# Optimization experiments

Hardware: AMD Instinct MI355X
Metric: run time of the kernel (lower is better)

## Reference

```python
import jax, jax.numpy as jnp
import numpy as np

B, S, HID = 128, 512, 512
IN_DIM = 1  # forced by x[:, t].unsqueeze(-1) + cat along dim 2


def setup_inputs() -> dict:
    key = jax.random.key(0)
    ks = jax.random.split(key, 9)
    scale = 0.05
    d_in = IN_DIM + HID
    return {
        "x": jax.random.normal(ks[0], (B, S, IN_DIM), dtype=jnp.float32),
        "H_prev": jnp.zeros((B, 1, HID), dtype=jnp.float32),
        "C_prev": jnp.zeros((B, 1, HID), dtype=jnp.float32),
        "Wi": jax.random.normal(ks[1], (d_in, HID), dtype=jnp.float32) * scale,
        "bi": jax.random.normal(ks[2], (1, HID), dtype=jnp.float32) * scale,
        "Wf": jax.random.normal(ks[3], (d_in, HID), dtype=jnp.float32) * scale,
        "bf": jax.random.normal(ks[4], (1, HID), dtype=jnp.float32) * scale,
        "Wc": jax.random.normal(ks[5], (d_in, HID), dtype=jnp.float32) * scale,
        "bc": jax.random.normal(ks[6], (1, HID), dtype=jnp.float32) * scale,
        "Wo": jax.random.normal(ks[7], (d_in, HID), dtype=jnp.float32) * scale,
        "bo": jax.random.normal(ks[8], (1, HID), dtype=jnp.float32) * scale,
    }


def reference(x, H_prev, C_prev, Wi, bi, Wf, bf, Wc, bc, Wo, bo):
    # x: [B, S, 1]; H_prev, C_prev: [B, 1, HID]
    def step(carry, x_t):
        H, C = carry  # each [B, 1, HID]
        comb = jnp.concatenate([x_t[:, None, :], H], axis=2)  # [B, 1, 1+HID]
        I = jax.nn.sigmoid(comb @ Wi + bi)
        F = jax.nn.sigmoid(comb @ Wf + bf)
        C_hat = jnp.tanh(comb @ Wc + bc)
        O = comb @ Wo + bo  # NOTE: no sigmoid, faithful to source
        C_new = F * C + I * C_hat
        H_new = O * jnp.tanh(C_new)
        return (H_new, C_new), None

    xs = jnp.swapaxes(x, 0, 1)  # [S, B, 1]
    (H_t, C_t), _ = jax.lax.scan(step, (H_prev, C_prev), xs)
    # original returns (hidden_sequence, H_t, C_t) where hidden_sequence == last H_t
    return (H_t, H_t, C_t)
```

## Files before the change

### kernel.cpp

```cpp
#include <hip/hip_runtime.h>
#include <math.h>

#define SEQ 512
#define HID 512
#define NGROUP 8
#define GB 16
#define BPG 32
#define SLOTU 65536
#define GSLOTU 8192
#define LROW 520

typedef __attribute__((ext_vector_type(8))) short short8;
typedef __attribute__((ext_vector_type(4))) float floatx4;

__device__ __forceinline__ unsigned short f2bf(float f) {
    unsigned u = __builtin_bit_cast(unsigned, f);
    return (unsigned short)((u + 0x7FFFu + ((u >> 16) & 1u)) >> 16);
}
__device__ __forceinline__ float bf2f(unsigned short h) {
    unsigned u = ((unsigned)h) << 16;
    return __builtin_bit_cast(float, u);
}
__device__ __forceinline__ float fast_sigmoid(float x) {
    return 1.0f / (1.0f + __expf(-x));
}
__device__ __forceinline__ float fast_tanh(float x) {
    float e = __expf(-2.0f * fabsf(x));
    float t = (1.0f - e) / (1.0f + e);
    return x < 0.0f ? -t : t;
}

__global__ void lstm_init(const float* __restrict__ H0, unsigned short* __restrict__ hb) {
    int idx = blockIdx.x * blockDim.x + threadIdx.x;
    if (idx < SLOTU) {
        int k = idx & 511, b = (idx >> 9) & 15, g = idx >> 13;
        hb[idx] = f2bf(H0[(g * GB + b) * HID + k]);
    } else if (idx < SLOTU + NGROUP * 64) {
        ((int*)(hb + 2 * SLOTU))[idx - SLOTU] = 0;
    }
}

__global__ __launch_bounds__(256, 1)
void lstm_main(const float* __restrict__ x,
               const float* __restrict__ C0,
               const float* __restrict__ Wi, const float* __restrict__ bi,
               const float* __restrict__ Wf, const float* __restrict__ bf_,
               const float* __restrict__ Wc, const float* __restrict__ bc,
               const float* __restrict__ Wo, const float* __restrict__ bo,
               float* __restrict__ out, unsigned short* __restrict__ hb) {
    int* flags = (int*)(hb + 2 * SLOTU);

    const int bid  = blockIdx.x;
    const int g    = bid & 7;
    const int cb   = bid >> 3;
    const int tid  = threadIdx.x;
    const int w    = tid >> 6;
    const int lane = tid & 63;
    const int q    = lane >> 4;
    const int c    = lane & 15;

    const int gate = c & 3;
    const int colA = cb * 16 + w * 4 + (c >> 2);
    const int colD = cb * 16 + w * 4 + q;
    const int bD   = g * GB + c;

    const float* Wg = (gate == 0) ? Wi : (gate == 1) ? Wf : (gate == 2) ? Wc : Wo;
    short8 aHi[16], aLo[16];
    #pragma unroll
    for (int kt = 0; kt < 16; ++kt) {
        #pragma unroll
        for (int j = 0; j < 8; ++j) {
            int k = kt * 32 + q * 8 + j;
            float wv = Wg[(k + 1) * HID + colA];
            unsigned short hi = f2bf(wv);
            unsigned short lo = f2bf(wv - bf2f(hi));
            aHi[kt][j] = (short)hi;
            aLo[kt][j] = (short)lo;
        }
    }

    const float biasI = bi[colD], biasF = bf_[colD], biasC = bc[colD], biasO = bo[colD];
    const float w0I = Wi[colD], w0F = Wf[colD], w0C = Wc[colD], w0O = Wo[colD];
    float Cst = C0[bD * HID + colD];
    const float* xrow = x + bD * SEQ;

    __shared__ unsigned short hlds[16 * LROW];

    int* myflag = flags + g * 64 + cb;

    for (int t = 0; t < SEQ; ++t) {
        if (tid < BPG) {
            const int* fp = flags + g * 64 + tid;
            while (__hip_atomic_load(fp, __ATOMIC_RELAXED, __HIP_MEMORY_SCOPE_AGENT) < t)
                __builtin_amdgcn_s_sleep(2);
        }
        __syncthreads();

        {
            const unsigned short* gsrc = hb + (t & 1) * SLOTU + g * GSLOTU + tid * 32;
            float4 v0, v1, v2, v3;
            asm volatile(
                "global_load_dwordx4 %0, %4, off sc0 sc1\n\t"
                "global_load_dwordx4 %1, %4, off offset:16 sc0 sc1\n\t"
                "global_load_dwordx4 %2, %4, off offset:32 sc0 sc1\n\t"
                "global_load_dwordx4 %3, %4, off offset:48 sc0 sc1\n\t"
                "s_waitcnt vmcnt(0)"
                : "=&v"(v0), "=&v"(v1), "=&v"(v2), "=&v"(v3)
                : "v"(gsrc) : "memory");
            int b = tid >> 4, ch = tid & 15;
            unsigned short* dst = hlds + b * LROW + ch * 32;
            *(float4*)(dst + 0)  = v0;
            *(float4*)(dst + 8)  = v1;
            *(float4*)(dst + 16) = v2;
            *(float4*)(dst + 24) = v3;
        }
        __syncthreads();

        floatx4 acc = {0.f, 0.f, 0.f, 0.f};
        const unsigned short* brow = hlds + c * LROW + q * 8;
        #pragma unroll
        for (int kt = 0; kt < 16; ++kt) {
            short8 bfrag = *(const short8*)(brow + kt * 32);
            acc = __builtin_amdgcn_mfma_f32_16x16x32_bf16(aHi[kt], bfrag, acc, 0, 0, 0);
            acc = __builtin_amdgcn_mfma_f32_16x16x32_bf16(aLo[kt], bfrag, acc, 0, 0, 0);
        }

        float xv  = xrow[t];
        float aIv = acc[0] + fmaf(xv, w0I, biasI);
        float aFv = acc[1] + fmaf(xv, w0F, biasF);
        float aCv = acc[2] + fmaf(xv, w0C, biasC);
        float aOv = acc[3] + fmaf(xv, w0O, biasO);
        float I  = fast_sigmoid(aIv);
        float F  = fast_sigmoid(aFv);
        float Ch = fast_tanh(aCv);
        Cst = fmaf(F, Cst, I * Ch);
        float Hn = aOv * fast_tanh(Cst);

        if (t < SEQ - 1) {
            int v = (int)f2bf(Hn);
            int o = __shfl_xor(v, 16);
            if ((q & 1) == 0) {
                unsigned val = (unsigned)(unsigned short)v |
                               ((unsigned)(unsigned short)o << 16);
                unsigned* dst = (unsigned*)(hb + ((t + 1) & 1) * SLOTU + g * GSLOTU
                                            + c * 512 + colD);
                __hip_atomic_store(dst, val, __ATOMIC_RELAXED, __HIP_MEMORY_SCOPE_AGENT);
            }
            __syncthreads();
            if (tid == 0)
                __hip_atomic_store(myflag, t + 1, __ATOMIC_RELAXED, __HIP_MEMORY_SCOPE_AGENT);
        } else {
            int o = bD * HID + colD;
            out[o] = Hn; out[65536 + o] = Hn; out[131072 + o] = Cst;
        }
    }
}

extern "C" void kernel_launch(void* const* d_in, const int* in_sizes, int n_in,
                              void* d_out, int out_size, void* d_ws, size_t ws_size,
                              hipStream_t stream) {
    const float* x  = (const float*)d_in[0];
    const float* H0 = (const float*)d_in[1];
    const float* C0 = (const float*)d_in[2];
    const float* Wi = (const float*)d_in[3];
    const float* bi = (const float*)d_in[4];
    const float* Wf = (const float*)d_in[5];
    const float* bf = (const float*)d_in[6];
    const float* Wc = (const float*)d_in[7];
    const float* bc = (const float*)d_in[8];
    const float* Wo = (const float*)d_in[9];
    const float* bo = (const float*)d_in[10];
    float* out = (float*)d_out;
    unsigned short* hb = (unsigned short*)d_ws;

    const int init_elems = SLOTU + NGROUP * 64;
    hipLaunchKernelGGL(lstm_init, dim3((init_elems + 255) / 256), dim3(256), 0, stream,
                       H0, hb);
    hipLaunchKernelGGL(lstm_main, dim3(NGROUP * BPG), dim3(256), 0, stream,
                       x, C0, Wi, bi, Wf, bf, Wc, bc, Wo, bo, out, hb);
}
```

Before: 1.389 ms.

## Replace per-block flags with step-tagged 64-bit hidden-state units

Removes the separate flag array and flag polling. Each 64-bit store now carries three bf16 hidden values plus the timestep in its top 16 bits. Consumers spin on the data loads themselves until every unit shows the expected tag, which drops one global round trip and a barrier from each step's critical path. In exchange the payload grows by a third, each reader does more and smaller loads with repacking into LDS, and correctness relies on 64-bit stores being single-copy atomic.

```diff
diff --git a/kernel.cpp b/kernel.cpp
--- a/kernel.cpp
+++ b/kernel.cpp
@@ -6,9 +6,9 @@
 #define NGROUP 8
 #define GB 16
 #define BPG 32
-#define SLOTU 65536
-#define GSLOTU 8192
 #define LROW 520
+#define UNITS_PER_GROUP 3072
+#define UNITS_PER_SLOT 24576
 
 typedef __attribute__((ext_vector_type(8))) short short8;
 typedef __attribute__((ext_vector_type(4))) float floatx4;
@@ -30,14 +30,21 @@
     return x < 0.0f ? -t : t;
 }
 
-__global__ void lstm_init(const float* __restrict__ H0, unsigned short* __restrict__ hb) {
+__global__ void lstm_init(const float* __restrict__ H0, unsigned long long* __restrict__ ub) {
     int idx = blockIdx.x * blockDim.x + threadIdx.x;
-    if (idx < SLOTU) {
-        int k = idx & 511, b = (idx >> 9) & 15, g = idx >> 13;
-        hb[idx] = f2bf(H0[(g * GB + b) * HID + k]);
-    } else if (idx < SLOTU + NGROUP * 64) {
-        ((int*)(hb + 2 * SLOTU))[idx - SLOTU] = 0;
-    }
+    if (idx >= UNITS_PER_SLOT) return;
+    int g   = idx / UNITS_PER_GROUP;
+    int rem = idx - g * UNITS_PER_GROUP;
+    int ci  = rem / 6;
+    int u   = rem - ci * 6;
+    int cb  = ci >> 4, b = ci & 15;
+    int row = (g * GB + b) * HID;
+    int c0  = cb * 16 + 3 * u;
+    int c1  = min(c0 + 1, 511), c2 = min(c0 + 2, 511);
+    unsigned long long v = (unsigned long long)f2bf(H0[row + c0])
+                         | ((unsigned long long)f2bf(H0[row + c1]) << 16)
+                         | ((unsigned long long)f2bf(H0[row + c2]) << 32);
+    ub[idx] = v;
 }
 
 __global__ __launch_bounds__(256, 1)
@@ -47,9 +54,7 @@
                const float* __restrict__ Wf, const float* __restrict__ bf_,
                const float* __restrict__ Wc, const float* __restrict__ bc,
                const float* __restrict__ Wo, const float* __restrict__ bo,
-               float* __restrict__ out, unsigned short* __restrict__ hb) {
-    int* flags = (int*)(hb + 2 * SLOTU);
-
+               float* __restrict__ out, unsigned long long* __restrict__ ub) {
     const int bid  = blockIdx.x;
     const int g    = bid & 7;
     const int cb   = bid >> 3;
@@ -85,34 +90,67 @@
     const float* xrow = x + bD * SEQ;
 
     __shared__ unsigned short hlds[16 * LROW];
-
-    int* myflag = flags + g * 64 + cb;
+    __shared__ unsigned short hout[16 * 16 + 2];
+
+    const int ciA = 2 * tid,      ciB = 2 * tid + 1;
+    const int ldsA = (ciA & 15) * LROW + (ciA >> 4) * 16;
+    const int ldsB = (ciB & 15) * LROW + (ciB >> 4) * 16;
+    const int punit = cb * 96 + tid;
+    const int pb16  = (tid / 6) * 16 + 3 * (tid - (tid / 6) * 6);
 
     for (int t = 0; t < SEQ; ++t) {
-        if (tid < BPG) {
-            const int* fp = flags + g * 64 + tid;
-            while (__hip_atomic_load(fp, __ATOMIC_RELAXED, __HIP_MEMORY_SCOPE_AGENT) < t)
-                __builtin_amdgcn_s_sleep(2);
-        }
-        __syncthreads();
+        const unsigned long long* up = ub + (t & 1) * UNITS_PER_SLOT
+                                          + g * UNITS_PER_GROUP + tid * 12;
+        const unsigned long long tg = (unsigned long long)t;
+        unsigned long long v0, v1, v2, v3, v4, v5, v6, v7, v8, v9, v10, v11;
+        while (1) {
+            asm volatile(
+                "global_load_dwordx2 %0, %12, off sc0 sc1\n\t"
+                "global_load_dwordx2 %1, %12, off offset:8 sc0 sc1\n\t"
+                "global_load_dwordx2 %2, %12, off offset:16 sc0 sc1\n\t"
+                "global_load_dwordx2 %3, %12, off offset:24 sc0 sc1\n\t"
+                "global_load_dwordx2 %4, %12, off offset:32 sc0 sc1\n\t"
+                "global_load_dwordx2 %5, %12, off offset:40 sc0 sc1\n\t"
+                "global_load_dwordx2 %6, %12, off offset:48 sc0 sc1\n\t"
+                "global_load_dwordx2 %7, %12, off offset:56 sc0 sc1\n\t"
+                "global_load_dwordx2 %8, %12, off offset:64 sc0 sc1\n\t"
+                "global_load_dwordx2 %9, %12, off offset:72 sc0 sc1\n\t"
+                "global_load_dwordx2 %10, %12, off offset:80 sc0 sc1\n\t"
+                "global_load_dwordx2 %11, %12, off offset:88 sc0 sc1\n\t"
+                "s_waitcnt vmcnt(0)"
+                : "=&v"(v0), "=&v"(v1), "=&v"(v2), "=&v"(v3), "=&v"(v4), "=&v"(v5),
+                  "=&v"(v6), "=&v"(v7), "=&v"(v8), "=&v"(v9), "=&v"(v10), "=&v"(v11)
+                : "v"(up) : "memory");
+            unsigned long long bad =
+                ((v0 >> 48) ^ tg) | ((v1 >> 48) ^ tg) | ((v2 >> 48) ^ tg) |
+                ((v3 >> 48) ^ tg) | ((v4 >> 48) ^ tg) | ((v5 >> 48) ^ tg) |
+                ((v6 >> 48) ^ tg) | ((v7 >> 48) ^ tg) | ((v8 >> 48) ^ tg) |
+                ((v9 >> 48) ^ tg) | ((v10 >> 48) ^ tg) | ((v11 >> 48) ^ tg);
+            if (bad == 0) break;
+            __builtin_amdgcn_s_sleep(1);
+        }
 
         {
-            const unsigned short* gsrc = hb + (t & 1) * SLOTU + g * GSLOTU + tid * 32;
-            float4 v0, v1, v2, v3;
-            asm volatile(
-                "global_load_dwordx4 %0, %4, off sc0 sc1\n\t"
-                "global_load_dwordx4 %1, %4, off offset:16 sc0 sc1\n\t"
-                "global_load_dwordx4 %2, %4, off offset:32 sc0 sc1\n\t"
-                "global_load_dwordx4 %3, %4, off offset:48 sc0 sc1\n\t"
-                "s_waitcnt vmcnt(0)"
-                : "=&v"(v0), "=&v"(v1), "=&v"(v2), "=&v"(v3)
-                : "v"(gsrc) : "memory");
-            int b = tid >> 4, ch = tid & 15;
-            unsigned short* dst = hlds + b * LROW + ch * 32;
-            *(float4*)(dst + 0)  = v0;
-            *(float4*)(dst + 8)  = v1;
-            *(float4*)(dst + 16) = v2;
-            *(float4*)(dst + 24) = v3;
+            unsigned d0 = (unsigned)v0;
+            unsigned d1 = (unsigned)((v0 >> 32) & 0xFFFF) | ((unsigned)(v1 & 0xFFFF) << 16);
+            unsigned d2 = (unsigned)(v1 >> 16);
+            unsigned d3 = (unsigned)v2;
+            unsigned d4 = (unsigned)((v2 >> 32) & 0xFFFF) | ((unsigned)(v3 & 0xFFFF) << 16);
+            unsigned d5 = (unsigned)(v3 >> 16);
+            unsigned d6 = (unsigned)v4;
+            unsigned d7 = (unsigned)((v4 >> 32) & 0xFFFF) | ((unsigned)(v5 & 0xFFFF) << 16);
+            *(uint4*)&hlds[ldsA]     = make_uint4(d0, d1, d2, d3);
+            *(uint4*)&hlds[ldsA + 8] = make_uint4(d4, d5, d6, d7);
+            unsigned e0 = (unsigned)v6;
+            unsigned e1 = (unsigned)((v6 >> 32) & 0xFFFF) | ((unsigned)(v7 & 0xFFFF) << 16);
+            unsigned e2 = (unsigned)(v7 >> 16);
+            unsigned e3 = (unsigned)v8;
+            unsigned e4 = (unsigned)((v8 >> 32) & 0xFFFF) | ((unsigned)(v9 & 0xFFFF) << 16);
+            unsigned e5 = (unsigned)(v9 >> 16);
+            unsigned e6 = (unsigned)v10;
+            unsigned e7 = (unsigned)((v10 >> 32) & 0xFFFF) | ((unsigned)(v11 & 0xFFFF) << 16);
+            *(uint4*)&hlds[ldsB]     = make_uint4(e0, e1, e2, e3);
+            *(uint4*)&hlds[ldsB + 8] = make_uint4(e4, e5, e6, e7);
         }
         __syncthreads();
 
@@ -137,18 +175,21 @@
         float Hn = aOv * fast_tanh(Cst);
 
         if (t < SEQ - 1) {
-            int v = (int)f2bf(Hn);
-            int o = __shfl_xor(v, 16);
-            if ((q & 1) == 0) {
-                unsigned val = (unsigned)(unsigned short)v |
-                               ((unsigned)(unsigned short)o << 16);
-                unsigned* dst = (unsigned*)(hb + ((t + 1) & 1) * SLOTU + g * GSLOTU
-                                            + c * 512 + colD);
-                __hip_atomic_store(dst, val, __ATOMIC_RELAXED, __HIP_MEMORY_SCOPE_AGENT);
+            hout[c * 16 + w * 4 + q] = f2bf(Hn);
+            __syncthreads();
+            if (tid < 96) {
+                unsigned long long val =
+                      (unsigned long long)hout[pb16]
+                    | ((unsigned long long)hout[pb16 + 1] << 16)
+                    | ((unsigned long long)hout[pb16 + 2] << 32)
+                    | ((unsigned long long)(t + 1) << 48);
+                unsigned long long* uptr = ub + ((t + 1) & 1) * UNITS_PER_SLOT
+                                              + g * UNITS_PER_GROUP + punit;
+                asm volatile(
+                    "global_store_dwordx2 %0, %1, off sc0 sc1\n\t"
+                    "s_waitcnt vmcnt(0)"
+                    :: "v"(uptr), "v"(val) : "memory");
             }
-            __syncthreads();
-            if (tid == 0)
-                __hip_atomic_store(myflag, t + 1, __ATOMIC_RELAXED, __HIP_MEMORY_SCOPE_AGENT);
         } else {
             int o = bD * HID + colD;
             out[o] = Hn; out[65536 + o] = Hn; out[131072 + o] = Cst;
@@ -171,11 +212,10 @@
     const float* Wo = (const float*)d_in[9];
     const float* bo = (const float*)d_in[10];
     float* out = (float*)d_out;
-    unsigned short* hb = (unsigned short*)d_ws;
-
-    const int init_elems = SLOTU + NGROUP * 64;
-    hipLaunchKernelGGL(lstm_init, dim3((init_elems + 255) / 256), dim3(256), 0, stream,
-                       H0, hb);
+    unsigned long long* ub = (unsigned long long*)d_ws;
+
+    hipLaunchKernelGGL(lstm_init, dim3(UNITS_PER_SLOT / 256), dim3(256), 0, stream,
+                       H0, ub);
     hipLaunchKernelGGL(lstm_main, dim3(NGROUP * BPG), dim3(256), 0, stream,
-                       x, C0, Wi, bi, Wf, bf, Wc, bc, Wo, bo, out, hb);
-}
+                       x, C0, Wi, bi, Wf, bf, Wc, bc, Wo, bo, out, ub);
+}
```

New measurement: 3.849 ms. +177.1%, slower.

## Use fp16 single-pass MFMA and fewer blocks per group with 64 columns each

Applied to the files above, without the earlier changes.

Replaces the split bf16 hi/lo weight representation with a single fp16 copy, halving the MFMA count per column. Each block now owns 64 hidden columns (4 MFMA tiles) instead of 16, so each batch group has 8 blocks instead of 32, which cuts the number of flags polled and the cross-block synchronization fan-in per timestep. The hidden-state output is staged in LDS and written with coalesced dwordx2 stores, and the flags are padded to separate cache lines. The trade-off is lower fp16 precision on weights and hidden state, more register pressure (64 half8 weight fragments), and fewer active CUs doing the per-step matvec.

```diff
diff --git a/kernel.cpp b/kernel.cpp
--- a/kernel.cpp
+++ b/kernel.cpp
@@ -5,22 +5,15 @@
 #define HID 512
 #define NGROUP 8
 #define GB 16
-#define BPG 32
-#define SLOTU 65536
-#define GSLOTU 8192
+#define BPG 8
+#define CPB 64
+#define SLOTH 65536
+#define GSLOT 8192
 #define LROW 520
 
-typedef __attribute__((ext_vector_type(8))) short short8;
-typedef __attribute__((ext_vector_type(4))) float floatx4;
+typedef _Float16 __attribute__((ext_vector_type(8))) half8;
+typedef float __attribute__((ext_vector_type(4))) floatx4;
 
-__device__ __forceinline__ unsigned short f2bf(float f) {
-    unsigned u = __builtin_bit_cast(unsigned, f);
-    return (unsigned short)((u + 0x7FFFu + ((u >> 16) & 1u)) >> 16);
-}
-__device__ __forceinline__ float bf2f(unsigned short h) {
-    unsigned u = ((unsigned)h) << 16;
-    return __builtin_bit_cast(float, u);
-}
 __device__ __forceinline__ float fast_sigmoid(float x) {
     return 1.0f / (1.0f + __expf(-x));
 }
@@ -30,13 +23,13 @@
     return x < 0.0f ? -t : t;
 }
 
-__global__ void lstm_init(const float* __restrict__ H0, unsigned short* __restrict__ hb) {
+__global__ void lstm_init(const float* __restrict__ H0, _Float16* __restrict__ hb) {
     int idx = blockIdx.x * blockDim.x + threadIdx.x;
-    if (idx < SLOTU) {
+    if (idx < SLOTH) {
         int k = idx & 511, b = (idx >> 9) & 15, g = idx >> 13;
-        hb[idx] = f2bf(H0[(g * GB + b) * HID + k]);
-    } else if (idx < SLOTU + NGROUP * 64) {
-        ((int*)(hb + 2 * SLOTU))[idx - SLOTU] = 0;
+        hb[idx] = (_Float16)H0[(g * GB + b) * HID + k];
+    } else if (idx < SLOTH + NGROUP * 128) {
+        ((int*)(hb + 2 * SLOTH))[idx - SLOTH] = 0;
     }
 }
 
@@ -47,8 +40,8 @@
                const float* __restrict__ Wf, const float* __restrict__ bf_,
                const float* __restrict__ Wc, const float* __restrict__ bc,
                const float* __restrict__ Wo, const float* __restrict__ bo,
-               float* __restrict__ out, unsigned short* __restrict__ hb) {
-    int* flags = (int*)(hb + 2 * SLOTU);
+               float* __restrict__ out, _Float16* __restrict__ hb) {
+    int* flags = (int*)(hb + 2 * SLOTH);
 
     const int bid  = blockIdx.x;
     const int g    = bid & 7;
@@ -59,45 +52,54 @@
     const int q    = lane >> 4;
     const int c    = lane & 15;
 
-    const int gate = c & 3;
-    const int colA = cb * 16 + w * 4 + (c >> 2);
-    const int colD = cb * 16 + w * 4 + q;
-    const int bD   = g * GB + c;
+    const int gate    = c & 3;
+    const int colbase = cb * CPB + w * 16;
+    const int bD      = g * GB + c;
 
     const float* Wg = (gate == 0) ? Wi : (gate == 1) ? Wf : (gate == 2) ? Wc : Wo;
-    short8 aHi[16], aLo[16];
+    half8 aW[4][16];
     #pragma unroll
-    for (int kt = 0; kt < 16; ++kt) {
+    for (int mt = 0; mt < 4; ++mt) {
+        const int colA = colbase + mt * 4 + (c >> 2);
         #pragma unroll
-        for (int j = 0; j < 8; ++j) {
-            int k = kt * 32 + q * 8 + j;
-            float wv = Wg[(k + 1) * HID + colA];
-            unsigned short hi = f2bf(wv);
-            unsigned short lo = f2bf(wv - bf2f(hi));
-            aHi[kt][j] = (short)hi;
-            aLo[kt][j] = (short)lo;
+        for (int kt = 0; kt < 16; ++kt) {
+            #pragma unroll
+            for (int j = 0; j < 8; ++j) {
+                int k = kt * 32 + q * 8 + j;
+                aW[mt][kt][j] = (_Float16)Wg[(k + 1) * HID + colA];
+            }
         }
     }
 
-    const float biasI = bi[colD], biasF = bf_[colD], biasC = bc[colD], biasO = bo[colD];
-    const float w0I = Wi[colD], w0F = Wf[colD], w0C = Wc[colD], w0O = Wo[colD];
-    float Cst = C0[bD * HID + colD];
+    float biasI[4], biasF[4], biasC[4], biasO[4];
+    float w0I[4], w0F[4], w0C[4], w0O[4], Cst[4];
+    #pragma unroll
+    for (int mt = 0; mt < 4; ++mt) {
+        int col = colbase + mt * 4 + q;
+        biasI[mt] = bi[col];  biasF[mt] = bf_[col];
+        biasC[mt] = bc[col];  biasO[mt] = bo[col];
+        w0I[mt] = Wi[col]; w0F[mt] = Wf[col]; w0C[mt] = Wc[col]; w0O[mt] = Wo[col];
+        Cst[mt] = C0[bD * HID + col];
+    }
     const float* xrow = x + bD * SEQ;
 
-    __shared__ unsigned short hlds[16 * LROW];
+    __shared__ _Float16 hlds[16 * LROW];
+    __shared__ _Float16 hout[16][64];
 
-    int* myflag = flags + g * 64 + cb;
+    int* myflag = flags + g * 128 + cb * 16;
 
     for (int t = 0; t < SEQ; ++t) {
+        float xv = xrow[t];
+
         if (tid < BPG) {
-            const int* fp = flags + g * 64 + tid;
+            const int* fp = flags + g * 128 + tid * 16;
             while (__hip_atomic_load(fp, __ATOMIC_RELAXED, __HIP_MEMORY_SCOPE_AGENT) < t)
-                __builtin_amdgcn_s_sleep(2);
+                __builtin_amdgcn_s_sleep(1);
         }
         __syncthreads();
 
         {
-            const unsigned short* gsrc = hb + (t & 1) * SLOTU + g * GSLOTU + tid * 32;
+            const _Float16* gsrc = hb + (t & 1) * SLOTH + g * GSLOT + tid * 32;
             float4 v0, v1, v2, v3;
             asm volatile(
                 "global_load_dwordx4 %0, %4, off sc0 sc1\n\t"
@@ -108,7 +110,7 @@
                 : "=&v"(v0), "=&v"(v1), "=&v"(v2), "=&v"(v3)
                 : "v"(gsrc) : "memory");
             int b = tid >> 4, ch = tid & 15;
-            unsigned short* dst = hlds + b * LROW + ch * 32;
+            _Float16* dst = hlds + b * LROW + ch * 32;
             *(float4*)(dst + 0)  = v0;
             *(float4*)(dst + 8)  = v1;
             *(float4*)(dst + 16) = v2;
@@ -116,42 +118,58 @@
         }
         __syncthreads();
 
-        floatx4 acc = {0.f, 0.f, 0.f, 0.f};
-        const unsigned short* brow = hlds + c * LROW + q * 8;
+        floatx4 acc[4] = {{0.f,0.f,0.f,0.f}, {0.f,0.f,0.f,0.f},
+                          {0.f,0.f,0.f,0.f}, {0.f,0.f,0.f,0.f}};
+        const _Float16* brow = hlds + c * LROW + q * 8;
         #pragma unroll
         for (int kt = 0; kt < 16; ++kt) {
-            short8 bfrag = *(const short8*)(brow + kt * 32);
-            acc = __builtin_amdgcn_mfma_f32_16x16x32_bf16(aHi[kt], bfrag, acc, 0, 0, 0);
-            acc = __builtin_amdgcn_mfma_f32_16x16x32_bf16(aLo[kt], bfrag, acc, 0, 0, 0);
+            half8 bfrag = *(const half8*)(brow + kt * 32);
+            #pragma unroll
+            for (int mt = 0; mt < 4; ++mt)
+                acc[mt] = __builtin_amdgcn_mfma_f32_16x16x32_f16(aW[mt][kt], bfrag,
+                                                                 acc[mt], 0, 0, 0);
         }
 
-        float xv  = xrow[t];
-        float aIv = acc[0] + fmaf(xv, w0I, biasI);
-        float aFv = acc[1] + fmaf(xv, w0F, biasF);
-        float aCv = acc[2] + fmaf(xv, w0C, biasC);
-        float aOv = acc[3] + fmaf(xv, w0O, biasO);
-        float I  = fast_sigmoid(aIv);
-        float F  = fast_sigmoid(aFv);
-        float Ch = fast_tanh(aCv);
-        Cst = fmaf(F, Cst, I * Ch);
-        float Hn = aOv * fast_tanh(Cst);
+        float Hn[4];
+        #pragma unroll
+        for (int mt = 0; mt < 4; ++mt) {
+            float aIv = acc[mt][0] + fmaf(xv, w0I[mt], biasI[mt]);
+            float aFv = acc[mt][1] + fmaf(xv, w0F[mt], biasF[mt]);
+            float aCv = acc[mt][2] + fmaf(xv, w0C[mt], biasC[mt]);
+            float aOv = acc[mt][3] + fmaf(xv, w0O[mt], biasO[mt]);
+            float I  = fast_sigmoid(aIv);
+            float F  = fast_sigmoid(aFv);
+            float Ch = fast_tanh(aCv);
+            Cst[mt] = fmaf(F, Cst[mt], I * Ch);
+            Hn[mt]  = aOv * fast_tanh(Cst[mt]);
+        }
 
         if (t < SEQ - 1) {
-            int v = (int)f2bf(Hn);
-            int o = __shfl_xor(v, 16);
-            if ((q & 1) == 0) {
-                unsigned val = (unsigned)(unsigned short)v |
-                               ((unsigned)(unsigned short)o << 16);
-                unsigned* dst = (unsigned*)(hb + ((t + 1) & 1) * SLOTU + g * GSLOTU
-                                            + c * 512 + colD);
-                __hip_atomic_store(dst, val, __ATOMIC_RELAXED, __HIP_MEMORY_SCOPE_AGENT);
+            #pragma unroll
+            for (int mt = 0; mt < 4; ++mt)
+                hout[c][w * 16 + mt * 4 + q] = (_Float16)Hn[mt];
+            __syncthreads();
+            if (tid < 128) {
+                int b = tid >> 3, ch = tid & 7;
+                unsigned long long s0 = *(const unsigned long long*)&hout[b][ch * 8];
+                unsigned long long s1 = *(const unsigned long long*)&hout[b][ch * 8 + 4];
+                _Float16* dst = hb + ((t + 1) & 1) * SLOTH + g * GSLOT
+                                + b * HID + cb * CPB + ch * 8;
+                asm volatile(
+                    "global_store_dwordx2 %0, %1, off sc0 sc1\n\t"
+                    "global_store_dwordx2 %0, %2, off offset:8 sc0 sc1\n\t"
+                    "s_waitcnt vmcnt(0)"
+                    :: "v"(dst), "v"(s0), "v"(s1) : "memory");
             }
             __syncthreads();
             if (tid == 0)
                 __hip_atomic_store(myflag, t + 1, __ATOMIC_RELAXED, __HIP_MEMORY_SCOPE_AGENT);
         } else {
-            int o = bD * HID + colD;
-            out[o] = Hn; out[65536 + o] = Hn; out[131072 + o] = Cst;
+            #pragma unroll
+            for (int mt = 0; mt < 4; ++mt) {
+                int o = bD * HID + colbase + mt * 4 + q;
+                out[o] = Hn[mt]; out[65536 + o] = Hn[mt]; out[131072 + o] = Cst[mt];
+            }
         }
     }
 }
@@ -171,9 +189,9 @@
     const float* Wo = (const float*)d_in[9];
     const float* bo = (const float*)d_in[10];
     float* out = (float*)d_out;
-    unsigned short* hb = (unsigned short*)d_ws;
+    _Float16* hb = (_Float16*)d_ws;
 
-    const int init_elems = SLOTU + NGROUP * 64;
+    const int init_elems = SLOTH + NGROUP * 128;
     hipLaunchKernelGGL(lstm_init, dim3((init_elems + 255) / 256), dim3(256), 0, stream,
                        H0, hb);
     hipLaunchKernelGGL(lstm_main, dim3(NGROUP * BPG), dim3(256), 0, stream,
```

Result: slower. 1.888 ms (+35.9%).

## Switch recurrent matmul from split bf16 to single fp16 MFMA with wider stores

Applied to the files above, without the earlier changes.

Replaces the hi/lo bf16 weight split (two MFMAs per k-tile) with a single fp16 weight fragment and fp16 hidden state, halving the MFMA work on the per-step critical path. Hidden-state publication now gathers four values per lane via shuffles and writes one 8-byte store with an explicit wait, instead of 4-byte atomic stores. The x load is hoisted before the spin-wait and the spin sleep is shortened. fp16 gives less dynamic range and a different precision profile than split bf16, which could affect accuracy across 512 recurrent steps.

```diff
diff --git a/kernel.cpp b/kernel.cpp
--- a/kernel.cpp
+++ b/kernel.cpp
@@ -6,21 +6,14 @@
 #define NGROUP 8
 #define GB 16
 #define BPG 32
-#define SLOTU 65536
-#define GSLOTU 8192
+#define CPB 16
+#define SLOTH 65536
+#define GSLOT 8192
 #define LROW 520
 
-typedef __attribute__((ext_vector_type(8))) short short8;
-typedef __attribute__((ext_vector_type(4))) float floatx4;
+typedef _Float16 __attribute__((ext_vector_type(8))) half8;
+typedef float __attribute__((ext_vector_type(4))) floatx4;
 
-__device__ __forceinline__ unsigned short f2bf(float f) {
-    unsigned u = __builtin_bit_cast(unsigned, f);
-    return (unsigned short)((u + 0x7FFFu + ((u >> 16) & 1u)) >> 16);
-}
-__device__ __forceinline__ float bf2f(unsigned short h) {
-    unsigned u = ((unsigned)h) << 16;
-    return __builtin_bit_cast(float, u);
-}
 __device__ __forceinline__ float fast_sigmoid(float x) {
     return 1.0f / (1.0f + __expf(-x));
 }
@@ -30,13 +23,13 @@
     return x < 0.0f ? -t : t;
 }
 
-__global__ void lstm_init(const float* __restrict__ H0, unsigned short* __restrict__ hb) {
+__global__ void lstm_init(const float* __restrict__ H0, _Float16* __restrict__ hb) {
     int idx = blockIdx.x * blockDim.x + threadIdx.x;
-    if (idx < SLOTU) {
+    if (idx < SLOTH) {
         int k = idx & 511, b = (idx >> 9) & 15, g = idx >> 13;
-        hb[idx] = f2bf(H0[(g * GB + b) * HID + k]);
-    } else if (idx < SLOTU + NGROUP * 64) {
-        ((int*)(hb + 2 * SLOTU))[idx - SLOTU] = 0;
+        hb[idx] = (_Float16)H0[(g * GB + b) * HID + k];
+    } else if (idx < SLOTH + NGROUP * 64) {
+        ((int*)(hb + 2 * SLOTH))[idx - SLOTH] = 0;
     }
 }
 
@@ -47,8 +40,8 @@
                const float* __restrict__ Wf, const float* __restrict__ bf_,
                const float* __restrict__ Wc, const float* __restrict__ bc,
                const float* __restrict__ Wo, const float* __restrict__ bo,
-               float* __restrict__ out, unsigned short* __restrict__ hb) {
-    int* flags = (int*)(hb + 2 * SLOTU);
+               float* __restrict__ out, _Float16* __restrict__ hb) {
+    int* flags = (int*)(hb + 2 * SLOTH);
 
     const int bid  = blockIdx.x;
     const int g    = bid & 7;
@@ -60,22 +53,18 @@
     const int c    = lane & 15;
 
     const int gate = c & 3;
-    const int colA = cb * 16 + w * 4 + (c >> 2);
-    const int colD = cb * 16 + w * 4 + q;
+    const int colA = cb * CPB + w * 4 + (c >> 2);
+    const int colD = cb * CPB + w * 4 + q;
     const int bD   = g * GB + c;
 
     const float* Wg = (gate == 0) ? Wi : (gate == 1) ? Wf : (gate == 2) ? Wc : Wo;
-    short8 aHi[16], aLo[16];
+    half8 aW[16];
     #pragma unroll
     for (int kt = 0; kt < 16; ++kt) {
         #pragma unroll
         for (int j = 0; j < 8; ++j) {
             int k = kt * 32 + q * 8 + j;
-            float wv = Wg[(k + 1) * HID + colA];
-            unsigned short hi = f2bf(wv);
-            unsigned short lo = f2bf(wv - bf2f(hi));
-            aHi[kt][j] = (short)hi;
-            aLo[kt][j] = (short)lo;
+            aW[kt][j] = (_Float16)Wg[(k + 1) * HID + colA];
         }
     }
 
@@ -84,20 +73,22 @@
     float Cst = C0[bD * HID + colD];
     const float* xrow = x + bD * SEQ;
 
-    __shared__ unsigned short hlds[16 * LROW];
+    __shared__ _Float16 hlds[16 * LROW];
 
     int* myflag = flags + g * 64 + cb;
 
     for (int t = 0; t < SEQ; ++t) {
+        float xv = xrow[t];
+
         if (tid < BPG) {
             const int* fp = flags + g * 64 + tid;
             while (__hip_atomic_load(fp, __ATOMIC_RELAXED, __HIP_MEMORY_SCOPE_AGENT) < t)
-                __builtin_amdgcn_s_sleep(2);
+                __builtin_amdgcn_s_sleep(1);
         }
         __syncthreads();
 
         {
-            const unsigned short* gsrc = hb + (t & 1) * SLOTU + g * GSLOTU + tid * 32;
+            const _Float16* gsrc = hb + (t & 1) * SLOTH + g * GSLOT + tid * 32;
             float4 v0, v1, v2, v3;
             asm volatile(
                 "global_load_dwordx4 %0, %4, off sc0 sc1\n\t"
@@ -108,7 +99,7 @@
                 : "=&v"(v0), "=&v"(v1), "=&v"(v2), "=&v"(v3)
                 : "v"(gsrc) : "memory");
             int b = tid >> 4, ch = tid & 15;
-            unsigned short* dst = hlds + b * LROW + ch * 32;
+            _Float16* dst = hlds + b * LROW + ch * 32;
             *(float4*)(dst + 0)  = v0;
             *(float4*)(dst + 8)  = v1;
             *(float4*)(dst + 16) = v2;
@@ -117,15 +108,13 @@
         __syncthreads();
 
         floatx4 acc = {0.f, 0.f, 0.f, 0.f};
-        const unsigned short* brow = hlds + c * LROW + q * 8;
+        const _Float16* brow = hlds + c * LROW + q * 8;
         #pragma unroll
         for (int kt = 0; kt < 16; ++kt) {
-            short8 bfrag = *(const short8*)(brow + kt * 32);
-            acc = __builtin_amdgcn_mfma_f32_16x16x32_bf16(aHi[kt], bfrag, acc, 0, 0, 0);
-            acc = __builtin_amdgcn_mfma_f32_16x16x32_bf16(aLo[kt], bfrag, acc, 0, 0, 0);
+            half8 bfrag = *(const half8*)(brow + kt * 32);
+            acc = __builtin_amdgcn_mfma_f32_16x16x32_f16(aW[kt], bfrag, acc, 0, 0, 0);
         }
 
-        float xv  = xrow[t];
         float aIv = acc[0] + fmaf(xv, w0I, biasI);
         float aFv = acc[1] + fmaf(xv, w0F, biasF);
         float aCv = acc[2] + fmaf(xv, w0C, biasC);
@@ -137,14 +126,22 @@
         float Hn = aOv * fast_tanh(Cst);
 
         if (t < SEQ - 1) {
-            int v = (int)f2bf(Hn);
-            int o = __shfl_xor(v, 16);
-            if ((q & 1) == 0) {
-                unsigned val = (unsigned)(unsigned short)v |
-                               ((unsigned)(unsigned short)o << 16);
-                unsigned* dst = (unsigned*)(hb + ((t + 1) & 1) * SLOTU + g * GSLOTU
-                                            + c * 512 + colD);
-                __hip_atomic_store(dst, val, __ATOMIC_RELAXED, __HIP_MEMORY_SCOPE_AGENT);
+            int hv = (int)__builtin_bit_cast(unsigned short, (_Float16)Hn);
+            int h1 = __shfl(hv, c + 16);
+            int h2 = __shfl(hv, c + 32);
+            int h3 = __shfl(hv, c + 48);
+            if (q == 0) {
+                unsigned long long val =
+                      (unsigned long long)(unsigned short)hv
+                    | ((unsigned long long)(unsigned short)h1 << 16)
+                    | ((unsigned long long)(unsigned short)h2 << 32)
+                    | ((unsigned long long)(unsigned short)h3 << 48);
+                _Float16* dst = hb + ((t + 1) & 1) * SLOTH + g * GSLOT
+                                + c * HID + cb * CPB + w * 4;
+                asm volatile(
+                    "global_store_dwordx2 %0, %1, off sc0 sc1\n\t"
+                    "s_waitcnt vmcnt(0)"
+                    :: "v"(dst), "v"(val) : "memory");
             }
             __syncthreads();
             if (tid == 0)
@@ -171,9 +168,9 @@
     const float* Wo = (const float*)d_in[9];
     const float* bo = (const float*)d_in[10];
     float* out = (float*)d_out;
-    unsigned short* hb = (unsigned short*)d_ws;
+    _Float16* hb = (_Float16*)d_ws;
 
-    const int init_elems = SLOTU + NGROUP * 64;
+    const int init_elems = SLOTH + NGROUP * 64;
     hipLaunchKernelGGL(lstm_init, dim3((init_elems + 255) / 256), dim3(256), 0, stream,
                        H0, hb);
     hipLaunchKernelGGL(lstm_main, dim3(NGROUP * BPG), dim3(256), 0, stream,
```

Result: slower. 1.695 ms (+22.0%).
